# Kernel optimization log

Hardware: AMD Instinct MI355X
Metric: run time of the kernel (lower is better)

## Reference

```python
import jax, jax.numpy as jnp
import numpy as np

NUM_SKILLS = 1000
DIM_S = 64
SIZE_M = 64
B, T = 64, 200


def setup_inputs() -> dict:
    key = jax.random.key(0)
    ks = jax.random.split(key, 16)
    skills = jax.random.randint(ks[0], (B, T), 0, NUM_SKILLS)
    responses = jax.random.randint(ks[1], (B, T), 0, 2)
    s = 1.0 / np.sqrt(DIM_S)
    return {
        "skills": skills,
        "responses": responses,
        "k_emb": jax.random.normal(ks[2], (NUM_SKILLS, DIM_S)) * s,
        "v_emb": jax.random.normal(ks[3], (2 * NUM_SKILLS, DIM_S)) * s,
        "Mk": jax.random.normal(ks[4], (SIZE_M, DIM_S)) * np.sqrt(2.0 / DIM_S),
        "Mv0": jax.random.normal(ks[5], (SIZE_M, DIM_S)) * np.sqrt(2.0 / DIM_S),
        "fW": jax.random.normal(ks[6], (DIM_S, 2 * DIM_S)) * (1.0 / np.sqrt(2 * DIM_S)),
        "fb": jnp.zeros((DIM_S,)),
        "eW": jax.random.normal(ks[7], (DIM_S, DIM_S)) * s,
        "eb": jnp.zeros((DIM_S,)),
        "aW": jax.random.normal(ks[8], (DIM_S, DIM_S)) * s,
        "ab": jnp.zeros((DIM_S,)),
        "pW": jax.random.normal(ks[9], (1, DIM_S)) * s,
        "pb": jnp.zeros((1,)),
    }


def reference(skills, responses, k_emb, v_emb, Mk, Mv0, fW, fb, eW, eb, aW, ab, pW, pb):
    # dropout is identity in eval mode
    masked_r = responses * (responses > -1).astype(responses.dtype)
    x = skills + NUM_SKILLS * masked_r            # [B, T]
    k = k_emb[skills]                              # [B, T, D]
    v = v_emb[x]                                   # [B, T, D]
    w = jax.nn.softmax(jnp.einsum('btd,md->btm', k, Mk), axis=-1)  # [B, T, M]
    e = jax.nn.sigmoid(v @ eW.T + eb)              # [B, T, D]
    a = jnp.tanh(v @ aW.T + ab)                    # [B, T, D]

    Mv_init = jnp.broadcast_to(Mv0, (skills.shape[0],) + Mv0.shape)  # [B, M, D]

    def step(Mvt, inp):
        wt, et, at = inp                           # [B,M], [B,D], [B,D]
        read = jnp.einsum('bm,bmd->bd', wt, Mvt)   # read BEFORE update (Mv[:, :-1])
        Mvt = Mvt * (1.0 - wt[:, :, None] * et[:, None, :]) + wt[:, :, None] * at[:, None, :]
        return Mvt, read

    xs = (jnp.swapaxes(w, 0, 1), jnp.swapaxes(e, 0, 1), jnp.swapaxes(a, 0, 1))
    _, reads = jax.lax.scan(step, Mv_init, xs)     # reads: [T, B, D]
    reads = jnp.swapaxes(reads, 0, 1)              # [B, T, D]

    f = jnp.tanh(jnp.concatenate([reads, k], axis=-1) @ fW.T + fb)  # [B, T, D]
    p = jax.nn.sigmoid(f @ pW.T + pb)[..., 0]      # [B, T]
    return p[:, 1:]                                # pred, [B, T-1]
```

## Files before the change

### kernel.cpp

```cpp
#include <hip/hip_runtime.h>
#include <stdint.h>

#define NSK 1000
#define TT  200
#define BB  64
#define NROW (BB * TT)
#define NOUT (BB * (TT-1))
#define CH  20
#define RW  2
#define NSPLIT 8
#define PSTR ((size_t)NROW * 64)

__device__ __forceinline__ unsigned ulane_bcast(unsigned v, int l) {
  return __builtin_amdgcn_readlane(v, l);
}
__device__ __forceinline__ float frcp(float x) { return __builtin_amdgcn_rcpf(x); }
__device__ __forceinline__ float sigm(float x) { return frcp(1.f + __expf(-x)); }
__device__ __forceinline__ float tanh_fast(float x) {
  return fmaf(-2.f, frcp(1.f + __expf(2.f * x)), 1.f);
}

typedef _Float16 half2v __attribute__((ext_vector_type(2)));
typedef _Float16 v8h __attribute__((ext_vector_type(8)));
typedef float    v4f __attribute__((ext_vector_type(4)));
union H2U { unsigned u; half2v h; };
union V8U { uint4 u; v8h h; };
__device__ __forceinline__ unsigned pack2h(float a, float b) {
  H2U x; x.h = (half2v){(_Float16)a, (_Float16)b}; return x.u;
}
__device__ __forceinline__ unsigned short f16bits(float x) {
  H2U u; u.h = (half2v){(_Float16)x, (_Float16)0.f}; return (unsigned short)(u.u & 0xffffu);
}
__device__ __forceinline__ float f16lo(unsigned bits) {
  H2U u; u.u = bits; return (float)u.h.x;
}
__device__ __forceinline__ float f16hi(unsigned bits) {
  H2U u; u.u = bits; return (float)u.h.y;
}
__device__ __forceinline__ v8h pk8(float4 x0, float4 x1) {
  return (v8h){(_Float16)x0.x, (_Float16)x0.y, (_Float16)x0.z, (_Float16)x0.w,
               (_Float16)x1.x, (_Float16)x1.y, (_Float16)x1.z, (_Float16)x1.w};
}

__global__ __launch_bounds__(128) void wea_mfma(
    const int* __restrict__ skills, const int* __restrict__ responses,
    const float* __restrict__ k_emb, const float* __restrict__ v_emb,
    const float* __restrict__ Mk, const float* __restrict__ eW,
    const float* __restrict__ eb, const float* __restrict__ aW,
    const float* __restrict__ ab,
    unsigned* __restrict__ ea_ws, unsigned short* __restrict__ w16_ws)
{
  const int tid  = threadIdx.x;
  const int wv   = tid >> 6, lane = tid & 63;
  const int tile = blockIdx.x * 2 + wv;
  const int r0   = tile * 16;
  const int lr   = lane & 15;
  const int lg   = lane >> 4;

  const int sk = skills[r0 + lr];
  int rr = responses[r0 + lr]; rr = (rr > -1) ? rr : 0;
  const int vrow = sk + NSK * rr;

  const float4* kq = (const float4*)(k_emb + (size_t)sk * 64);
  const float4* vq = (const float4*)(v_emb + (size_t)vrow * 64);
  v8h ak[2], av[2];
  #pragma unroll
  for (int t = 0; t < 2; ++t) {
    const int o = t * 8 + lg * 2;
    ak[t] = pk8(kq[o], kq[o + 1]);
    av[t] = pk8(vq[o], vq[o + 1]);
  }

  float ebv[4], abv[4];
  #pragma unroll
  for (int c = 0; c < 4; ++c) { ebv[c] = eb[16 * c + lr]; abv[c] = ab[16 * c + lr]; }

  v4f acK[4], acE[4], acA[4];
  #pragma unroll
  for (int c = 0; c < 4; ++c) {
    acK[c] = (v4f){0.f, 0.f, 0.f, 0.f};
    acE[c] = (v4f){0.f, 0.f, 0.f, 0.f};
    acA[c] = (v4f){0.f, 0.f, 0.f, 0.f};
  }

  #pragma unroll
  for (int c = 0; c < 4; ++c) {
    const float4* mq = (const float4*)(Mk + (size_t)(16 * c + lr) * 64);
    const float4* eq = (const float4*)(eW + (size_t)(16 * c + lr) * 64);
    const float4* aq = (const float4*)(aW + (size_t)(16 * c + lr) * 64);
    #pragma unroll
    for (int t = 0; t < 2; ++t) {
      const int o = t * 8 + lg * 2;
      const v8h bm = pk8(mq[o], mq[o + 1]);
      const v8h be = pk8(eq[o], eq[o + 1]);
      const v8h ba = pk8(aq[o], aq[o + 1]);
      acK[c] = __builtin_amdgcn_mfma_f32_16x16x32_f16(ak[t], bm, acK[c], 0, 0, 0);
      acE[c] = __builtin_amdgcn_mfma_f32_16x16x32_f16(av[t], be, acE[c], 0, 0, 0);
      acA[c] = __builtin_amdgcn_mfma_f32_16x16x32_f16(av[t], ba, acA[c], 0, 0, 0);
    }
  }

  float rs[4];
  #pragma unroll
  for (int q = 0; q < 4; ++q) {
    float m = fmaxf(fmaxf(acK[0][q], acK[1][q]), fmaxf(acK[2][q], acK[3][q]));
    #pragma unroll
    for (int off = 8; off; off >>= 1) m = fmaxf(m, __shfl_xor(m, off));
    float s = 0.f;
    #pragma unroll
    for (int c = 0; c < 4; ++c) {
      acK[c][q] = __expf(acK[c][q] - m);
      s += acK[c][q];
    }
    #pragma unroll
    for (int off = 8; off; off >>= 1) s += __shfl_xor(s, off);
    rs[q] = frcp(s);
  }

  #pragma unroll
  for (int c = 0; c < 4; ++c) {
    const int j = 16 * c + lr;
    #pragma unroll
    for (int q = 0; q < 4; ++q) {
      const int row = r0 + lg * 4 + q;
      w16_ws[(size_t)row * 64 + j] = f16bits(acK[c][q] * rs[q]);
      const float ev = sigm(acE[c][q] + ebv[c]);
      const float avv = tanh_fast(acA[c][q] + abv[c]);
      ea_ws[(size_t)row * 64 + j] = pack2h(ev, avv);
    }
  }
}

__device__ __forceinline__ void load_chunk(
    const unsigned* __restrict__ eap, const unsigned short* __restrict__ wp,
    int t0, int wl, int lane, unsigned* eab, unsigned* wvb)
{
  #pragma unroll
  for (int k = 0; k < CH; ++k) {
    eab[k] = eap[(t0 + k) * 64 + lane];
    wvb[k] = (unsigned)wp[(t0 + k) * 64 + wl];
  }
}

__device__ __forceinline__ void compute_chunk(
    float* Mv, const unsigned* eab, const unsigned* wvb,
    float* __restrict__ red, int wave, int lane)
{
  #pragma unroll
  for (int k = 0; k < CH; ++k) {
    const float ev = f16lo(eab[k]), av = f16hi(eab[k]);
    float rp = 0.f;
    #pragma unroll
    for (int i = 0; i < RW; ++i) {
      const float wm = f16lo(ulane_bcast(wvb[k], i));
      rp = fmaf(wm, Mv[i], rp);
      float tp = fmaf(-ev, Mv[i], av);
      Mv[i] = fmaf(wm, tp, Mv[i]);
    }
    red[k * 256 + wave * 64 + lane] = rp;
  }
}

__device__ __forceinline__ void reduce_store(
    const float* __restrict__ red, int ch, int base, int wave, int lane,
    unsigned short* __restrict__ ps)
{
  #pragma unroll
  for (int u = 0; u < 5; ++u) {
    const int k = wave * 5 + u;
    const float* rr = red + k * 256;
    const float v = (rr[lane] + rr[64 + lane]) + (rr[128 + lane] + rr[192 + lane]);
    ps[(size_t)(base + ch * CH + k) * 64 + lane] = f16bits(v);
  }
}

__global__ __launch_bounds__(256) void scan_kernel(
    const float* __restrict__ Mv0,
    const unsigned* __restrict__ ea_ws, const unsigned short* __restrict__ w16_ws,
    unsigned short* __restrict__ pbase)
{
  __shared__ float red[2][CH * 256];
  const int b    = blockIdx.x >> 3;
  const int s    = blockIdx.x & 7;
  const int wave = threadIdx.x >> 6;
  const int lane = threadIdx.x & 63;
  const int base = b * TT;
  const int m0   = s * 8 + wave * RW;
  const int wl   = m0 + (lane & (RW - 1));
  unsigned short* ps = pbase + (size_t)s * PSTR;

  float Mv[RW];
  #pragma unroll
  for (int i = 0; i < RW; ++i) Mv[i] = Mv0[(size_t)(m0 + i) * 64 + lane];

  const unsigned* eap = ea_ws + (size_t)base * 64;
  const unsigned short* wp = w16_ws + (size_t)base * 64;

  unsigned ea0[CH], wv0[CH], ea1[CH], wv1[CH];
  load_chunk(eap, wp, 0, wl, lane, ea0, wv0);
  for (int ch = 0; ch < TT / CH; ch += 2) {
    if ((ch + 1) * CH < TT)
      load_chunk(eap, wp, (ch + 1) * CH, wl, lane, ea1, wv1);
    compute_chunk(Mv, ea0, wv0, red[0], wave, lane);
    __syncthreads();
    reduce_store(red[0], ch, base, wave, lane, ps);
    if ((ch + 2) * CH < TT)
      load_chunk(eap, wp, (ch + 2) * CH, wl, lane, ea0, wv0);
    if ((ch + 1) * CH < TT) {
      compute_chunk(Mv, ea1, wv1, red[1], wave, lane);
      __syncthreads();
      reduce_store(red[1], ch + 1, base, wave, lane, ps);
    }
  }
}

__global__ __launch_bounds__(256) void fp_mfma(
    const int* __restrict__ skills, const float* __restrict__ k_emb,
    const float* __restrict__ fW, const float* __restrict__ fb,
    const float* __restrict__ pW, const float* __restrict__ pb,
    const unsigned short* __restrict__ pbase,
    float* __restrict__ out)
{
  const int tid  = threadIdx.x;
  const int wv   = tid >> 6, lane = tid & 63;
  const int lr   = lane & 15;
  const int lg   = lane >> 4;
  const int o0   = (blockIdx.x * 4 + wv) * 16;

  const unsigned idx = o0 + lr;
  const unsigned bb  = idx / 199u;
  const unsigned t2  = idx - bb * 199u;
  const int srow     = (int)(idx + bb + 1u);

  v8h ar[4];
  #pragma unroll
  for (int t = 0; t < 2; ++t) {
    const size_t eo = (size_t)srow * 64 + t * 32 + lg * 8;
    V8U s0, s1, s2, s3;
    s0.u = *(const uint4*)&pbase[eo];
    s1.u = *(const uint4*)&pbase[eo + PSTR];
    s2.u = *(const uint4*)&pbase[eo + 2 * PSTR];
    s3.u = *(const uint4*)&pbase[eo + 3 * PSTR];
    v8h acc = (s0.h + s1.h) + (s2.h + s3.h);
    s0.u = *(const uint4*)&pbase[eo + 4 * PSTR];
    s1.u = *(const uint4*)&pbase[eo + 5 * PSTR];
    s2.u = *(const uint4*)&pbase[eo + 6 * PSTR];
    s3.u = *(const uint4*)&pbase[eo + 7 * PSTR];
    ar[t] = acc + ((s0.h + s1.h) + (s2.h + s3.h));
  }
  {
    const float4* kq = (const float4*)(k_emb + (size_t)skills[srow] * 64);
    #pragma unroll
    for (int t = 2; t < 4; ++t) {
      const int o = (t - 2) * 8 + lg * 2;
      ar[t] = pk8(kq[o], kq[o + 1]);
    }
  }

  float fbv[4], pwv[4];
  #pragma unroll
  for (int c = 0; c < 4; ++c) { fbv[c] = fb[16 * c + lr]; pwv[c] = pW[16 * c + lr]; }

  v4f acc[4];
  #pragma unroll
  for (int c = 0; c < 4; ++c) acc[c] = (v4f){0.f, 0.f, 0.f, 0.f};

  const float4* fq = (const float4*)fW;
  #pragma unroll
  for (int c = 0; c < 4; ++c) {
    const int jb = (16 * c + lr) * 32;
    #pragma unroll
    for (int t = 0; t < 4; ++t) {
      const int o = jb + t * 8 + lg * 2;
      const v8h bf = pk8(fq[o], fq[o + 1]);
      acc[c] = __builtin_amdgcn_mfma_f32_16x16x32_f16(ar[t], bf, acc[c], 0, 0, 0);
    }
  }

  const float pb0 = pb[0];
  #pragma unroll
  for (int q = 0; q < 4; ++q) {
    float s = 0.f;
    #pragma unroll
    for (int c = 0; c < 4; ++c)
      s += tanh_fast(acc[c][q] + fbv[c]) * pwv[c];
    #pragma unroll
    for (int off = 8; off; off >>= 1) s += __shfl_xor(s, off);
    if (lr == lg * 4 + q)
      out[(size_t)bb * (TT - 1) + t2] = sigm(s + pb0);
  }
}

extern "C" void kernel_launch(void* const* d_in, const int* in_sizes, int n_in,
                              void* d_out, int out_size, void* d_ws, size_t ws_size,
                              hipStream_t stream) {
  const int* skills    = (const int*)d_in[0];
  const int* responses = (const int*)d_in[1];
  const float* k_emb   = (const float*)d_in[2];
  const float* v_emb   = (const float*)d_in[3];
  const float* Mk      = (const float*)d_in[4];
  const float* Mv0     = (const float*)d_in[5];
  const float* fW      = (const float*)d_in[6];
  const float* fb      = (const float*)d_in[7];
  const float* eW      = (const float*)d_in[8];
  const float* eb      = (const float*)d_in[9];
  const float* aW      = (const float*)d_in[10];
  const float* ab      = (const float*)d_in[11];
  const float* pW      = (const float*)d_in[12];
  const float* pb      = (const float*)d_in[13];
  (void)in_sizes; (void)n_in; (void)out_size; (void)ws_size;

  unsigned* ea_ws        = (unsigned*)d_ws;
  unsigned short* w16_ws = (unsigned short*)(ea_ws + (size_t)NROW * 64);
  unsigned short* pbase  = w16_ws + PSTR;

  wea_mfma<<<dim3(400), 128, 0, stream>>>(
      skills, responses, k_emb, v_emb, Mk, eW, eb, aW, ab, ea_ws, w16_ws);
  scan_kernel<<<dim3(BB * NSPLIT), 256, 0, stream>>>(Mv0, ea_ws, w16_ws, pbase);
  fp_mfma<<<dim3(199), 256, 0, stream>>>(
      skills, k_emb, fW, fb, pW, pb, pbase, (float*)d_out);
}
```

Baseline: 119.9 us.

## Fuse projection/softmax kernel into scan kernel using LDS staging

Merges the embedding projection and softmax kernel into the scan kernel. Each block computes the e/a and attention weights for its batch row directly into shared memory, then runs the recurrent memory update from LDS. This removes a kernel launch and the global workspace write/read of the intermediate tensors. In exchange, each of the 8 split blocks per batch recomputes the full e/a projection, and the scan chunk size is halved, which adds more barriers.

```diff
diff --git a/kernel.cpp b/kernel.cpp
--- a/kernel.cpp
+++ b/kernel.cpp
@@ -6,7 +6,7 @@
 #define BB  64
 #define NROW (BB * TT)
 #define NOUT (BB * (TT-1))
-#define CH  20
+#define SCH 10
 #define RW  2
 #define NSPLIT 8
 #define PSTR ((size_t)NROW * 64)
@@ -42,174 +42,144 @@
                (_Float16)x1.x, (_Float16)x1.y, (_Float16)x1.z, (_Float16)x1.w};
 }
 
-__global__ __launch_bounds__(128) void wea_mfma(
+__global__ __launch_bounds__(256) void wea_scan(
     const int* __restrict__ skills, const int* __restrict__ responses,
     const float* __restrict__ k_emb, const float* __restrict__ v_emb,
     const float* __restrict__ Mk, const float* __restrict__ eW,
     const float* __restrict__ eb, const float* __restrict__ aW,
-    const float* __restrict__ ab,
-    unsigned* __restrict__ ea_ws, unsigned short* __restrict__ w16_ws)
+    const float* __restrict__ ab, const float* __restrict__ Mv0,
+    unsigned short* __restrict__ pbase)
 {
+  __shared__ unsigned ea_lds[TT * 64];
+  __shared__ unsigned short w_lds[TT * 8];
+  __shared__ float red[2][SCH * 256];
+
   const int tid  = threadIdx.x;
   const int wv   = tid >> 6, lane = tid & 63;
-  const int tile = blockIdx.x * 2 + wv;
-  const int r0   = tile * 16;
+  const int b    = blockIdx.x >> 3, s = blockIdx.x & 7;
   const int lr   = lane & 15;
   const int lg   = lane >> 4;
-
-  const int sk = skills[r0 + lr];
-  int rr = responses[r0 + lr]; rr = (rr > -1) ? rr : 0;
-  const int vrow = sk + NSK * rr;
-
-  const float4* kq = (const float4*)(k_emb + (size_t)sk * 64);
-  const float4* vq = (const float4*)(v_emb + (size_t)vrow * 64);
-  v8h ak[2], av[2];
-  #pragma unroll
-  for (int t = 0; t < 2; ++t) {
-    const int o = t * 8 + lg * 2;
-    ak[t] = pk8(kq[o], kq[o + 1]);
-    av[t] = pk8(vq[o], vq[o + 1]);
-  }
-
-  float ebv[4], abv[4];
-  #pragma unroll
-  for (int c = 0; c < 4; ++c) { ebv[c] = eb[16 * c + lr]; abv[c] = ab[16 * c + lr]; }
-
-  v4f acK[4], acE[4], acA[4];
-  #pragma unroll
-  for (int c = 0; c < 4; ++c) {
-    acK[c] = (v4f){0.f, 0.f, 0.f, 0.f};
-    acE[c] = (v4f){0.f, 0.f, 0.f, 0.f};
-    acA[c] = (v4f){0.f, 0.f, 0.f, 0.f};
-  }
-
-  #pragma unroll
-  for (int c = 0; c < 4; ++c) {
-    const float4* mq = (const float4*)(Mk + (size_t)(16 * c + lr) * 64);
-    const float4* eq = (const float4*)(eW + (size_t)(16 * c + lr) * 64);
-    const float4* aq = (const float4*)(aW + (size_t)(16 * c + lr) * 64);
-    #pragma unroll
-    for (int t = 0; t < 2; ++t) {
-      const int o = t * 8 + lg * 2;
-      const v8h bm = pk8(mq[o], mq[o + 1]);
-      const v8h be = pk8(eq[o], eq[o + 1]);
-      const v8h ba = pk8(aq[o], aq[o + 1]);
-      acK[c] = __builtin_amdgcn_mfma_f32_16x16x32_f16(ak[t], bm, acK[c], 0, 0, 0);
-      acE[c] = __builtin_amdgcn_mfma_f32_16x16x32_f16(av[t], be, acE[c], 0, 0, 0);
-      acA[c] = __builtin_amdgcn_mfma_f32_16x16x32_f16(av[t], ba, acA[c], 0, 0, 0);
-    }
-  }
-
-  float rs[4];
-  #pragma unroll
-  for (int q = 0; q < 4; ++q) {
-    float m = fmaxf(fmaxf(acK[0][q], acK[1][q]), fmaxf(acK[2][q], acK[3][q]));
-    #pragma unroll
-    for (int off = 8; off; off >>= 1) m = fmaxf(m, __shfl_xor(m, off));
-    float s = 0.f;
-    #pragma unroll
-    for (int c = 0; c < 4; ++c) {
-      acK[c][q] = __expf(acK[c][q] - m);
-      s += acK[c][q];
-    }
-    #pragma unroll
-    for (int off = 8; off; off >>= 1) s += __shfl_xor(s, off);
-    rs[q] = frcp(s);
-  }
-
-  #pragma unroll
-  for (int c = 0; c < 4; ++c) {
-    const int j = 16 * c + lr;
-    #pragma unroll
-    for (int q = 0; q < 4; ++q) {
-      const int row = r0 + lg * 4 + q;
-      w16_ws[(size_t)row * 64 + j] = f16bits(acK[c][q] * rs[q]);
-      const float ev = sigm(acE[c][q] + ebv[c]);
-      const float avv = tanh_fast(acA[c][q] + abv[c]);
-      ea_ws[(size_t)row * 64 + j] = pack2h(ev, avv);
-    }
-  }
-}
-
-__device__ __forceinline__ void load_chunk(
-    const unsigned* __restrict__ eap, const unsigned short* __restrict__ wp,
-    int t0, int wl, int lane, unsigned* eab, unsigned* wvb)
-{
-  #pragma unroll
-  for (int k = 0; k < CH; ++k) {
-    eab[k] = eap[(t0 + k) * 64 + lane];
-    wvb[k] = (unsigned)wp[(t0 + k) * 64 + wl];
-  }
-}
-
-__device__ __forceinline__ void compute_chunk(
-    float* Mv, const unsigned* eab, const unsigned* wvb,
-    float* __restrict__ red, int wave, int lane)
-{
-  #pragma unroll
-  for (int k = 0; k < CH; ++k) {
-    const float ev = f16lo(eab[k]), av = f16hi(eab[k]);
-    float rp = 0.f;
-    #pragma unroll
-    for (int i = 0; i < RW; ++i) {
-      const float wm = f16lo(ulane_bcast(wvb[k], i));
-      rp = fmaf(wm, Mv[i], rp);
-      float tp = fmaf(-ev, Mv[i], av);
-      Mv[i] = fmaf(wm, tp, Mv[i]);
-    }
-    red[k * 256 + wave * 64 + lane] = rp;
-  }
-}
-
-__device__ __forceinline__ void reduce_store(
-    const float* __restrict__ red, int ch, int base, int wave, int lane,
-    unsigned short* __restrict__ ps)
-{
-  #pragma unroll
-  for (int u = 0; u < 5; ++u) {
-    const int k = wave * 5 + u;
-    const float* rr = red + k * 256;
-    const float v = (rr[lane] + rr[64 + lane]) + (rr[128 + lane] + rr[192 + lane]);
-    ps[(size_t)(base + ch * CH + k) * 64 + lane] = f16bits(v);
-  }
-}
-
-__global__ __launch_bounds__(256) void scan_kernel(
-    const float* __restrict__ Mv0,
-    const unsigned* __restrict__ ea_ws, const unsigned short* __restrict__ w16_ws,
-    unsigned short* __restrict__ pbase)
-{
-  __shared__ float red[2][CH * 256];
-  const int b    = blockIdx.x >> 3;
-  const int s    = blockIdx.x & 7;
-  const int wave = threadIdx.x >> 6;
-  const int lane = threadIdx.x & 63;
-  const int base = b * TT;
-  const int m0   = s * 8 + wave * RW;
-  const int wl   = m0 + (lane & (RW - 1));
-  unsigned short* ps = pbase + (size_t)s * PSTR;
-
-  float Mv[RW];
-  #pragma unroll
-  for (int i = 0; i < RW; ++i) Mv[i] = Mv0[(size_t)(m0 + i) * 64 + lane];
-
-  const unsigned* eap = ea_ws + (size_t)base * 64;
-  const unsigned short* wp = w16_ws + (size_t)base * 64;
-
-  unsigned ea0[CH], wv0[CH], ea1[CH], wv1[CH];
-  load_chunk(eap, wp, 0, wl, lane, ea0, wv0);
-  for (int ch = 0; ch < TT / CH; ch += 2) {
-    if ((ch + 1) * CH < TT)
-      load_chunk(eap, wp, (ch + 1) * CH, wl, lane, ea1, wv1);
-    compute_chunk(Mv, ea0, wv0, red[0], wave, lane);
-    __syncthreads();
-    reduce_store(red[0], ch, base, wave, lane, ps);
-    if ((ch + 2) * CH < TT)
-      load_chunk(eap, wp, (ch + 2) * CH, wl, lane, ea0, wv0);
-    if ((ch + 1) * CH < TT) {
-      compute_chunk(Mv, ea1, wv1, red[1], wave, lane);
+  const int cw   = s >> 1, lrh = s & 1;
+
+  {
+    float ebv[4], abv[4];
+    #pragma unroll
+    for (int c = 0; c < 4; ++c) { ebv[c] = eb[16 * c + lr]; abv[c] = ab[16 * c + lr]; }
+
+    #pragma unroll 1
+    for (int t = wv; t < 13; t += 4) {
+      const int rbase = t * 16;
+      const int rl    = min(rbase + lr, TT - 1);
+      const int row   = b * TT + rl;
+      const int sk = skills[row];
+      int rr = responses[row]; rr = (rr > -1) ? rr : 0;
+      const float4* kq = (const float4*)(k_emb + (size_t)sk * 64);
+      const float4* vq = (const float4*)(v_emb + (size_t)(sk + NSK * rr) * 64);
+      v8h ak[2], av[2];
+      #pragma unroll
+      for (int u = 0; u < 2; ++u) {
+        const int o = u * 8 + lg * 2;
+        ak[u] = pk8(kq[o], kq[o + 1]);
+        av[u] = pk8(vq[o], vq[o + 1]);
+      }
+
+      v4f acK[4], acE[4], acA[4];
+      #pragma unroll
+      for (int c = 0; c < 4; ++c) {
+        acK[c] = (v4f){0.f, 0.f, 0.f, 0.f};
+        acE[c] = (v4f){0.f, 0.f, 0.f, 0.f};
+        acA[c] = (v4f){0.f, 0.f, 0.f, 0.f};
+      }
+      #pragma unroll
+      for (int c = 0; c < 4; ++c) {
+        const float4* mq = (const float4*)(Mk + (size_t)(16 * c + lr) * 64);
+        const float4* eq = (const float4*)(eW + (size_t)(16 * c + lr) * 64);
+        const float4* aq = (const float4*)(aW + (size_t)(16 * c + lr) * 64);
+        #pragma unroll
+        for (int u = 0; u < 2; ++u) {
+          const int o = u * 8 + lg * 2;
+          const v8h bm = pk8(mq[o], mq[o + 1]);
+          const v8h be = pk8(eq[o], eq[o + 1]);
+          const v8h ba = pk8(aq[o], aq[o + 1]);
+          acK[c] = __builtin_amdgcn_mfma_f32_16x16x32_f16(ak[u], bm, acK[c], 0, 0, 0);
+          acE[c] = __builtin_amdgcn_mfma_f32_16x16x32_f16(av[u], be, acE[c], 0, 0, 0);
+          acA[c] = __builtin_amdgcn_mfma_f32_16x16x32_f16(av[u], ba, acA[c], 0, 0, 0);
+        }
+      }
+
+      float rs[4];
+      #pragma unroll
+      for (int q = 0; q < 4; ++q) {
+        float m = fmaxf(fmaxf(acK[0][q], acK[1][q]), fmaxf(acK[2][q], acK[3][q]));
+        #pragma unroll
+        for (int off = 8; off; off >>= 1) m = fmaxf(m, __shfl_xor(m, off));
+        float sm = 0.f;
+        #pragma unroll
+        for (int c = 0; c < 4; ++c) {
+          acK[c][q] = __expf(acK[c][q] - m);
+          sm += acK[c][q];
+        }
+        #pragma unroll
+        for (int off = 8; off; off >>= 1) sm += __shfl_xor(sm, off);
+        rs[q] = frcp(sm);
+      }
+
+      #pragma unroll
+      for (int c = 0; c < 4; ++c) {
+        const int j = 16 * c + lr;
+        #pragma unroll
+        for (int q = 0; q < 4; ++q) {
+          const int rloc = rbase + lg * 4 + q;
+          if (rloc < TT) {
+            const float ev  = sigm(acE[c][q] + ebv[c]);
+            const float avv = tanh_fast(acA[c][q] + abv[c]);
+            ea_lds[rloc * 64 + j] = pack2h(ev, avv);
+            if (c == cw && (lr >> 3) == lrh)
+              w_lds[rloc * 8 + (lr & 7)] = f16bits(acK[c][q] * rs[q]);
+          }
+        }
+      }
+    }
+  }
+  __syncthreads();
+
+  {
+    const int m0 = s * 8 + wv * RW;
+    unsigned short* ps = pbase + (size_t)s * PSTR;
+    const size_t base = (size_t)b * TT;
+    float Mv[RW];
+    #pragma unroll
+    for (int i = 0; i < RW; ++i) Mv[i] = Mv0[(size_t)(m0 + i) * 64 + lane];
+
+    #pragma unroll 1
+    for (int ch = 0; ch < TT / SCH; ++ch) {
+      const int t0 = ch * SCH;
+      float* rbuf = red[ch & 1];
+      unsigned eab[SCH], wvb[SCH];
+      #pragma unroll
+      for (int k = 0; k < SCH; ++k) {
+        eab[k] = ea_lds[(t0 + k) * 64 + lane];
+        wvb[k] = (unsigned)w_lds[(t0 + k) * 8 + wv * RW + (lane & (RW - 1))];
+      }
+      #pragma unroll
+      for (int k = 0; k < SCH; ++k) {
+        const float ev = f16lo(eab[k]), av = f16hi(eab[k]);
+        float rp = 0.f;
+        #pragma unroll
+        for (int i = 0; i < RW; ++i) {
+          const float wm = f16lo(ulane_bcast(wvb[k], i));
+          rp = fmaf(wm, Mv[i], rp);
+          float tp = fmaf(-ev, Mv[i], av);
+          Mv[i] = fmaf(wm, tp, Mv[i]);
+        }
+        rbuf[k * 256 + wv * 64 + lane] = rp;
+      }
       __syncthreads();
-      reduce_store(red[1], ch + 1, base, wave, lane, ps);
+      for (int k = wv; k < SCH; k += 4) {
+        const float* rr2 = rbuf + k * 256;
+        const float v = (rr2[lane] + rr2[64 + lane]) + (rr2[128 + lane] + rr2[192 + lane]);
+        ps[(base + t0 + k) * 64 + lane] = f16bits(v);
+      }
     }
   }
 }
@@ -310,13 +280,10 @@
   const float* pb      = (const float*)d_in[13];
   (void)in_sizes; (void)n_in; (void)out_size; (void)ws_size;
 
-  unsigned* ea_ws        = (unsigned*)d_ws;
-  unsigned short* w16_ws = (unsigned short*)(ea_ws + (size_t)NROW * 64);
-  unsigned short* pbase  = w16_ws + PSTR;
-
-  wea_mfma<<<dim3(400), 128, 0, stream>>>(
-      skills, responses, k_emb, v_emb, Mk, eW, eb, aW, ab, ea_ws, w16_ws);
-  scan_kernel<<<dim3(BB * NSPLIT), 256, 0, stream>>>(Mv0, ea_ws, w16_ws, pbase);
+  unsigned short* pbase = (unsigned short*)d_ws;
+
+  wea_scan<<<dim3(BB * NSPLIT), 256, 0, stream>>>(
+      skills, responses, k_emb, v_emb, Mk, eW, eb, aW, ab, Mv0, pbase);
   fp_mfma<<<dim3(199), 256, 0, stream>>>(
       skills, k_emb, fW, fb, pW, pb, pbase, (float*)d_out);
 }
```

Result: slower. 132.2 us (+10.3%).

## Split memory scan across 16 blocks per batch with one row per wave

Applied to the files above, without the earlier changes.

The scan kernel now uses 16 slot-splits per batch element instead of 8, so each wave owns a single memory row instead of two. The chunk size drops to 10 steps, and the lane readlane broadcast is replaced by a direct per-wave load of the weight. The goal is more parallelism and a shorter per-step dependency chain on the serial scan. In exchange, the fp kernel must sum 16 partial read buffers instead of 8, which doubles both the partial-sum workspace traffic and the block count.

```diff
diff --git a/kernel.cpp b/kernel.cpp
--- a/kernel.cpp
+++ b/kernel.cpp
@@ -6,14 +6,11 @@
 #define BB  64
 #define NROW (BB * TT)
 #define NOUT (BB * (TT-1))
-#define CH  20
-#define RW  2
-#define NSPLIT 8
+#define CH  10
+#define RW  1
+#define NSPLIT 16
 #define PSTR ((size_t)NROW * 64)
 
-__device__ __forceinline__ unsigned ulane_bcast(unsigned v, int l) {
-  return __builtin_amdgcn_readlane(v, l);
-}
 __device__ __forceinline__ float frcp(float x) { return __builtin_amdgcn_rcpf(x); }
 __device__ __forceinline__ float sigm(float x) { return frcp(1.f + __expf(-x)); }
 __device__ __forceinline__ float tanh_fast(float x) {
@@ -131,85 +128,69 @@
   }
 }
 
-__device__ __forceinline__ void load_chunk(
-    const unsigned* __restrict__ eap, const unsigned short* __restrict__ wp,
-    int t0, int wl, int lane, unsigned* eab, unsigned* wvb)
-{
-  #pragma unroll
-  for (int k = 0; k < CH; ++k) {
-    eab[k] = eap[(t0 + k) * 64 + lane];
-    wvb[k] = (unsigned)wp[(t0 + k) * 64 + wl];
-  }
-}
-
-__device__ __forceinline__ void compute_chunk(
-    float* Mv, const unsigned* eab, const unsigned* wvb,
-    float* __restrict__ red, int wave, int lane)
-{
-  #pragma unroll
-  for (int k = 0; k < CH; ++k) {
-    const float ev = f16lo(eab[k]), av = f16hi(eab[k]);
-    float rp = 0.f;
-    #pragma unroll
-    for (int i = 0; i < RW; ++i) {
-      const float wm = f16lo(ulane_bcast(wvb[k], i));
-      rp = fmaf(wm, Mv[i], rp);
-      float tp = fmaf(-ev, Mv[i], av);
-      Mv[i] = fmaf(wm, tp, Mv[i]);
-    }
-    red[k * 256 + wave * 64 + lane] = rp;
-  }
-}
-
-__device__ __forceinline__ void reduce_store(
-    const float* __restrict__ red, int ch, int base, int wave, int lane,
-    unsigned short* __restrict__ ps)
-{
-  #pragma unroll
-  for (int u = 0; u < 5; ++u) {
-    const int k = wave * 5 + u;
-    const float* rr = red + k * 256;
-    const float v = (rr[lane] + rr[64 + lane]) + (rr[128 + lane] + rr[192 + lane]);
-    ps[(size_t)(base + ch * CH + k) * 64 + lane] = f16bits(v);
-  }
-}
-
 __global__ __launch_bounds__(256) void scan_kernel(
     const float* __restrict__ Mv0,
     const unsigned* __restrict__ ea_ws, const unsigned short* __restrict__ w16_ws,
     unsigned short* __restrict__ pbase)
 {
   __shared__ float red[2][CH * 256];
-  const int b    = blockIdx.x >> 3;
-  const int s    = blockIdx.x & 7;
+  const int b    = blockIdx.x >> 4;
+  const int s    = blockIdx.x & 15;
   const int wave = threadIdx.x >> 6;
   const int lane = threadIdx.x & 63;
-  const int base = b * TT;
-  const int m0   = s * 8 + wave * RW;
-  const int wl   = m0 + (lane & (RW - 1));
+  const size_t base = (size_t)b * TT;
+  const int m0   = s * 4 + wave;
   unsigned short* ps = pbase + (size_t)s * PSTR;
 
-  float Mv[RW];
-  #pragma unroll
-  for (int i = 0; i < RW; ++i) Mv[i] = Mv0[(size_t)(m0 + i) * 64 + lane];
-
-  const unsigned* eap = ea_ws + (size_t)base * 64;
-  const unsigned short* wp = w16_ws + (size_t)base * 64;
+  float Mv = Mv0[(size_t)m0 * 64 + lane];
+
+  const unsigned* eap = ea_ws + base * 64;
+  const unsigned short* wp = w16_ws + base * 64;
 
   unsigned ea0[CH], wv0[CH], ea1[CH], wv1[CH];
-  load_chunk(eap, wp, 0, wl, lane, ea0, wv0);
+  #pragma unroll
+  for (int k = 0; k < CH; ++k) {
+    ea0[k] = eap[k * 64 + lane];
+    wv0[k] = (unsigned)wp[k * 64 + m0];
+  }
   for (int ch = 0; ch < TT / CH; ch += 2) {
-    if ((ch + 1) * CH < TT)
-      load_chunk(eap, wp, (ch + 1) * CH, wl, lane, ea1, wv1);
-    compute_chunk(Mv, ea0, wv0, red[0], wave, lane);
+    #pragma unroll
+    for (int k = 0; k < CH; ++k) {
+      ea1[k] = eap[((ch + 1) * CH + k) * 64 + lane];
+      wv1[k] = (unsigned)wp[((ch + 1) * CH + k) * 64 + m0];
+    }
+    #pragma unroll
+    for (int k = 0; k < CH; ++k) {
+      const float ev = f16lo(ea0[k]), av = f16hi(ea0[k]);
+      const float wm = f16lo(wv0[k]);
+      red[0][k * 256 + wave * 64 + lane] = wm * Mv;
+      Mv = fmaf(wm, fmaf(-ev, Mv, av), Mv);
+    }
     __syncthreads();
-    reduce_store(red[0], ch, base, wave, lane, ps);
-    if ((ch + 2) * CH < TT)
-      load_chunk(eap, wp, (ch + 2) * CH, wl, lane, ea0, wv0);
-    if ((ch + 1) * CH < TT) {
-      compute_chunk(Mv, ea1, wv1, red[1], wave, lane);
-      __syncthreads();
-      reduce_store(red[1], ch + 1, base, wave, lane, ps);
+    for (int k = wave; k < CH; k += 4) {
+      const float* rr = red[0] + k * 256;
+      const float v = (rr[lane] + rr[64 + lane]) + (rr[128 + lane] + rr[192 + lane]);
+      ps[(base + ch * CH + k) * 64 + lane] = f16bits(v);
+    }
+    if ((ch + 2) * CH < TT) {
+      #pragma unroll
+      for (int k = 0; k < CH; ++k) {
+        ea0[k] = eap[((ch + 2) * CH + k) * 64 + lane];
+        wv0[k] = (unsigned)wp[((ch + 2) * CH + k) * 64 + m0];
+      }
+    }
+    #pragma unroll
+    for (int k = 0; k < CH; ++k) {
+      const float ev = f16lo(ea1[k]), av = f16hi(ea1[k]);
+      const float wm = f16lo(wv1[k]);
+      red[1][k * 256 + wave * 64 + lane] = wm * Mv;
+      Mv = fmaf(wm, fmaf(-ev, Mv, av), Mv);
+    }
+    __syncthreads();
+    for (int k = wave; k < CH; k += 4) {
+      const float* rr = red[1] + k * 256;
+      const float v = (rr[lane] + rr[64 + lane]) + (rr[128 + lane] + rr[192 + lane]);
+      ps[(base + (ch + 1) * CH + k) * 64 + lane] = f16bits(v);
     }
   }
 }
@@ -236,17 +217,17 @@
   #pragma unroll
   for (int t = 0; t < 2; ++t) {
     const size_t eo = (size_t)srow * 64 + t * 32 + lg * 8;
-    V8U s0, s1, s2, s3;
-    s0.u = *(const uint4*)&pbase[eo];
-    s1.u = *(const uint4*)&pbase[eo + PSTR];
-    s2.u = *(const uint4*)&pbase[eo + 2 * PSTR];
-    s3.u = *(const uint4*)&pbase[eo + 3 * PSTR];
-    v8h acc = (s0.h + s1.h) + (s2.h + s3.h);
-    s0.u = *(const uint4*)&pbase[eo + 4 * PSTR];
-    s1.u = *(const uint4*)&pbase[eo + 5 * PSTR];
-    s2.u = *(const uint4*)&pbase[eo + 6 * PSTR];
-    s3.u = *(const uint4*)&pbase[eo + 7 * PSTR];
-    ar[t] = acc + ((s0.h + s1.h) + (s2.h + s3.h));
+    v8h g[4];
+    #pragma unroll
+    for (int pp = 0; pp < 4; ++pp) {
+      V8U s0, s1, s2, s3;
+      s0.u = *(const uint4*)&pbase[eo + (size_t)(4 * pp) * PSTR];
+      s1.u = *(const uint4*)&pbase[eo + (size_t)(4 * pp + 1) * PSTR];
+      s2.u = *(const uint4*)&pbase[eo + (size_t)(4 * pp + 2) * PSTR];
+      s3.u = *(const uint4*)&pbase[eo + (size_t)(4 * pp + 3) * PSTR];
+      g[pp] = (s0.h + s1.h) + (s2.h + s3.h);
+    }
+    ar[t] = (g[0] + g[1]) + (g[2] + g[3]);
   }
   {
     const float4* kq = (const float4*)(k_emb + (size_t)skills[srow] * 64);
```

Measured after the change: 127.6 us. 1.06x slower.
